# Performance work log

Measured on AMD Instinct MI355X. Metric: run time of the kernel, lower is better.

Reference implementation:

```python
import jax, jax.numpy as jnp
import numpy as np


def setup_inputs() -> dict:
    key = jax.random.key(0)
    x = jax.random.normal(key, (64, 3, 224, 224), dtype=jnp.float32)
    return {"x": x, "patch_size": 16, "overlap": 8}


def reference(x, patch_size, overlap):
    # x: [B, C, H, H]
    B, C, H, _ = x.shape
    stride = patch_size - overlap
    assert (H - patch_size) % stride == 0, 'adjust the patch_size and the overlap_size!'
    n = (H - patch_size) // stride + 1  # patch_num per spatial dim
    # window row/col indices: [n, p]
    idx = jnp.arange(n)[:, None] * stride + jnp.arange(patch_size)[None, :]
    # gather rows then cols in one vectorized pass (no Python loop over patches)
    rows = x[:, :, idx, :]            # [B, C, n, p, H]
    patches = rows[:, :, :, :, idx]   # [B, C, n, p, n, p]
    # b c h d1 w d2 -> b h w c d1 d2
    patches = patches.transpose(0, 2, 4, 1, 3, 5)
    # b h w c d1 d2 -> b (h w) c (d1 d2)
    return patches.reshape(B, n * n, C, patch_size * patch_size)
```

## Files before the change

### kernel.cpp

```cpp
#include <hip/hip_runtime.h>


constexpr int NB    = 64;
constexpr int NC    = 3;
constexpr int HW    = 224;
constexpr int PS    = 16;
constexpr int ST    = 8;
constexpr int NP    = 27;
constexpr int NPP   = NP * NP;
constexpr int TPB   = NC * (PS * PS / 4);

__global__ __launch_bounds__(TPB) void overlap_patch_kernel(
    const float4* __restrict__ x, float4* __restrict__ out)
{
    const int bp = blockIdx.x;
    const int p  = bp % NPP;
    const int b  = bp / NPP;
    const int py = p / NP;
    const int px = p % NP;

    const int t  = threadIdx.x;
    const int c  = t >> 6;
    const int q4 = t & 63;
    const int r  = q4 >> 2;
    const int s  = (q4 & 3) << 2;

    const int row = py * ST + r;
    const int col = px * ST + s;
    const long in_elem = ((long)(b * NC + c) * HW + row) * HW + col;

    out[(long)bp * TPB + t] = x[in_elem >> 2];
}

extern "C" void kernel_launch(void* const* d_in, const int* in_sizes, int n_in,
                              void* d_out, int out_size, void* d_ws, size_t ws_size,
                              hipStream_t stream) {
    const float4* x = (const float4*)d_in[0];
    float4* out = (float4*)d_out;
    const int grid = NB * NPP;
    overlap_patch_kernel<<<grid, TPB, 0, stream>>>(x, out);
}
```

Before: 193.0 us.

## Stage patch row strips in LDS and emit all patches per block

```diff
diff --git a/kernel.cpp b/kernel.cpp
--- a/kernel.cpp
+++ b/kernel.cpp
@@ -1,35 +1,55 @@
 #include <hip/hip_runtime.h>
 
 
-constexpr int NB    = 64;
-constexpr int NC    = 3;
-constexpr int HW    = 224;
-constexpr int PS    = 16;
-constexpr int ST    = 8;
-constexpr int NP    = 27;
-constexpr int NPP   = NP * NP;
-constexpr int TPB   = NC * (PS * PS / 4);
+constexpr int NB  = 64;
+constexpr int NC  = 3;
+constexpr int HWD = 224;
+constexpr int PS  = 16;
+constexpr int ST  = 8;
+constexpr int NP  = 27;
+constexpr int ROW4 = HWD / 4;
+constexpr int LDSW = 228;
+constexpr int TPB  = 256;
 
-__global__ __launch_bounds__(TPB) void overlap_patch_kernel(
+__global__ __launch_bounds__(TPB) void overlap_patch_lds(
     const float4* __restrict__ x, float4* __restrict__ out)
 {
-    const int bp = blockIdx.x;
-    const int p  = bp % NPP;
-    const int b  = bp / NPP;
-    const int py = p / NP;
-    const int px = p % NP;
+    const int blk = blockIdx.x;
+    const int c   = blk % NC;
+    const int tmp = blk / NC;
+    const int py  = tmp % NP;
+    const int b   = tmp / NP;
 
-    const int t  = threadIdx.x;
-    const int c  = t >> 6;
-    const int q4 = t & 63;
-    const int r  = q4 >> 2;
-    const int s  = (q4 & 3) << 2;
+    __shared__ float lds[PS * LDSW];
 
-    const int row = py * ST + r;
-    const int col = px * ST + s;
-    const long in_elem = ((long)(b * NC + c) * HW + row) * HW + col;
+    const int t = threadIdx.x;
 
-    out[(long)bp * TPB + t] = x[in_elem >> 2];
+    const int gbase = ((b * NC + c) * HWD + py * ST) * ROW4;
+    #pragma unroll
+    for (int k = 0; k < 4; ++k) {
+        const int j = t + k * TPB;
+        if (j < PS * ROW4) {
+            const int r    = j / ROW4;
+            const int col4 = j - r * ROW4;
+            const float4 v = x[gbase + j];
+            *(float4*)&lds[r * LDSW + col4 * 4] = v;
+        }
+    }
+    __syncthreads();
+
+    const int obase = ((b * NP * NP + py * NP) * NC + c) * 64;
+    #pragma unroll
+    for (int k = 0; k < 7; ++k) {
+        const int j = t + k * TPB;
+        if (j < NP * 64) {
+            const int px = j >> 6;
+            const int q4 = j & 63;
+            const int r  = q4 >> 2;
+            const int s  = (q4 & 3) << 2;
+            const float4 v = *(const float4*)&lds[r * LDSW + px * ST + s];
+            out[obase + px * (NC * 64) + q4] = v;
+        }
+    }
 }
 
 extern "C" void kernel_launch(void* const* d_in, const int* in_sizes, int n_in,
@@ -37,6 +57,6 @@
                               hipStream_t stream) {
     const float4* x = (const float4*)d_in[0];
     float4* out = (float4*)d_out;
-    const int grid = NB * NPP;
-    overlap_patch_kernel<<<grid, TPB, 0, stream>>>(x, out);
+    const int grid = NB * NP * NC;
+    overlap_patch_lds<<<grid, TPB, 0, stream>>>(x, out);
 }
```

New measurement: 173.8 us. 1.11x faster.
